# Optimization experiments

Hardware: AMD Instinct MI355X
Metric: run time of the kernel (lower is better)

Reference implementation:

```python
import jax, jax.numpy as jnp
import numpy as np


def setup_inputs() -> dict:
    key = jax.random.key(0)
    kK, kQ = jax.random.split(key)
    B, S, D = 8, 2048, 512
    K = jax.random.normal(kK, (B, S, D), dtype=jnp.float32)
    Q = jax.random.normal(kQ, (B, S, D), dtype=jnp.float32)
    return {"K": K, "Q": Q}


def reference(K, Q):
    # K: [B, S_k, D], Q: [B, S_q, D]
    S_q = Q.shape[1]
    S_k = K.shape[1]
    # Causal mask: -inf strictly above the diagonal (k=1), as in np.triu(..., k=1)
    mask = jnp.where(jnp.triu(jnp.ones((S_q, S_k), dtype=bool), k=1), -jnp.inf, 0.0).astype(jnp.float32)
    # NOTE: original scales by sqrt(window_size_keys) (seq len), and adds mask BEFORE scaling.
    logits = (jnp.einsum('bqd,bkd->bqk', Q, K) + mask) / jnp.sqrt(jnp.float32(S_k))
    return jax.nn.softmax(logits, axis=-1)
```

## Files before the change

kernel.cpp:

```cpp
#include <hip/hip_runtime.h>
#include <hip/hip_bf16.h>
#include <math.h>

#define B_SZ 8
#define SEQ 2048
#define DIM 512

typedef __attribute__((ext_vector_type(8))) short bf16x8;
typedef __attribute__((ext_vector_type(8))) unsigned short u16x8;
typedef __attribute__((ext_vector_type(4))) float f32x4;

#define GLOBAL_AS __attribute__((address_space(1)))
#define LDS_AS __attribute__((address_space(3)))

__device__ __forceinline__ unsigned short f2bf(float f) {
    unsigned int u = __builtin_bit_cast(unsigned int, f);
    u += 0x7fffu + ((u >> 16) & 1u);
    return (unsigned short)(u >> 16);
}

__device__ __forceinline__ void load_lds16(const void* g, void* l) {
    __builtin_amdgcn_global_load_lds((const GLOBAL_AS unsigned int*)g,
                                     (LDS_AS unsigned int*)l, 16, 0, 0);
}

__global__ __launch_bounds__(256)
void convert_kernel(const float* __restrict__ src, unsigned short* __restrict__ dst) {
    int i = blockIdx.x * 256 + threadIdx.x;
    const float4* s = (const float4*)src;
    float4 a = s[2 * i];
    float4 b = s[2 * i + 1];
    u16x8 o;
    o[0] = f2bf(a.x); o[1] = f2bf(a.y); o[2] = f2bf(a.z); o[3] = f2bf(a.w);
    o[4] = f2bf(b.x); o[5] = f2bf(b.y); o[6] = f2bf(b.z); o[7] = f2bf(b.w);
    ((u16x8*)dst)[i] = o;
}

#define BM 128
#define BK 32
__global__ __launch_bounds__(256)
void logits_mfma(const unsigned short* __restrict__ Qb, const unsigned short* __restrict__ Kb,
                 float* __restrict__ out) {
    const int tk = blockIdx.x, tq = blockIdx.y, b = blockIdx.z;
    if (tk > tq) return;

    __shared__ __align__(16) unsigned short a_lds[BM * BK];
    __shared__ __align__(16) unsigned short b_lds[BM * BK];

    const int t = threadIdx.x;
    const int wave = t >> 6;
    const int lane = t & 63;
    const int l16 = lane & 15;
    const int quad = lane >> 4;
    const int wm = wave >> 1;
    const int wn = wave & 1;

    const unsigned short* Qrow = Qb + ((size_t)b * SEQ + (size_t)tq * BM) * DIM;
    const unsigned short* Krow = Kb + ((size_t)b * SEQ + (size_t)tk * BM) * DIM;

    const int sr = lane >> 2;
    const int kg = lane & 3;

    f32x4 acc[4][4];
#pragma unroll
    for (int i = 0; i < 4; i++)
#pragma unroll
        for (int j = 0; j < 4; j++) acc[i][j] = (f32x4){0.f, 0.f, 0.f, 0.f};

    for (int k0 = 0; k0 < DIM; k0 += BK) {
#pragma unroll
        for (int j = wave; j < 8; j += 4) {
            int row = j * 16 + sr;
            load_lds16(Qrow + (size_t)row * DIM + k0 + kg * 8, &a_lds[(j * 16) * BK]);
            load_lds16(Krow + (size_t)row * DIM + k0 + kg * 8, &b_lds[(j * 16) * BK]);
        }
        __syncthreads();

        bf16x8 af[4], bf[4];
#pragma unroll
        for (int mi = 0; mi < 4; mi++)
            af[mi] = *(const bf16x8*)&a_lds[(wm * 64 + mi * 16 + l16) * BK + quad * 8];
#pragma unroll
        for (int ni = 0; ni < 4; ni++)
            bf[ni] = *(const bf16x8*)&b_lds[(wn * 64 + ni * 16 + l16) * BK + quad * 8];
#pragma unroll
        for (int mi = 0; mi < 4; mi++)
#pragma unroll
            for (int ni = 0; ni < 4; ni++)
                acc[mi][ni] = __builtin_amdgcn_mfma_f32_16x16x32_bf16(af[mi], bf[ni], acc[mi][ni], 0, 0, 0);
        __syncthreads();
    }

    const float scale = 0.02209708691207961f;
    float* outb = out + (size_t)b * SEQ * SEQ;
#pragma unroll
    for (int mi = 0; mi < 4; mi++) {
#pragma unroll
        for (int ni = 0; ni < 4; ni++) {
            int col = tk * BM + wn * 64 + ni * 16 + l16;
#pragma unroll
            for (int r = 0; r < 4; r++) {
                int row = tq * BM + wm * 64 + mi * 16 + quad * 4 + r;
                outb[(size_t)row * SEQ + col] = acc[mi][ni][r] * scale;
            }
        }
    }
}

__global__ __launch_bounds__(256)
void softmax_kernel(float* __restrict__ out) {
    const int q = blockIdx.x & (SEQ - 1);
    const int b = blockIdx.x >> 11;
    float* row = out + ((size_t)b * SEQ + q) * SEQ;
    const int t = threadIdx.x;
    const int lane = t & 63;
    const int wave = t >> 6;
    const int n = q + 1;

    __shared__ float red[8];

    float4 v[2];
    float m = -INFINITY;
#pragma unroll
    for (int j = 0; j < 2; j++) {
        int k0 = (t + j * 256) * 4;
        if (k0 < n) {
            float4 x = *(const float4*)(row + k0);
            x.y = (k0 + 1 < n) ? x.y : -INFINITY;
            x.z = (k0 + 2 < n) ? x.z : -INFINITY;
            x.w = (k0 + 3 < n) ? x.w : -INFINITY;
            v[j] = x;
            m = fmaxf(m, fmaxf(fmaxf(x.x, x.y), fmaxf(x.z, x.w)));
        } else {
            v[j] = (float4){-INFINITY, -INFINITY, -INFINITY, -INFINITY};
        }
    }
#pragma unroll
    for (int off = 1; off < 64; off <<= 1) m = fmaxf(m, __shfl_xor(m, off));
    if (lane == 0) red[wave] = m;
    __syncthreads();
    m = fmaxf(fmaxf(red[0], red[1]), fmaxf(red[2], red[3]));

    float s = 0.f;
#pragma unroll
    for (int j = 0; j < 2; j++) {
        float4 e;
        e.x = __expf(v[j].x - m);
        e.y = __expf(v[j].y - m);
        e.z = __expf(v[j].z - m);
        e.w = __expf(v[j].w - m);
        v[j] = e;
        s += e.x + e.y + e.z + e.w;
    }
#pragma unroll
    for (int off = 1; off < 64; off <<= 1) s += __shfl_xor(s, off);
    if (lane == 0) red[4 + wave] = s;
    __syncthreads();
    s = red[4] + red[5] + red[6] + red[7];
    const float inv = 1.0f / s;

#pragma unroll
    for (int j = 0; j < 2; j++) {
        int k0 = (t + j * 256) * 4;
        float4 e = v[j];
        e.x *= inv; e.y *= inv; e.z *= inv; e.w *= inv;
        *(float4*)(row + k0) = e;
    }
}

#define TS 64
#define DC 128
#define LSTRIDE (DC + 8)
__global__ __launch_bounds__(256)
void logits_fallback(const float* __restrict__ Q, const float* __restrict__ K,
                     float* __restrict__ out) {
    const int tk = blockIdx.x, tq = blockIdx.y, b = blockIdx.z;
    if (tk > tq) return;
    __shared__ __align__(16) unsigned short qs[TS * LSTRIDE];
    __shared__ __align__(16) unsigned short ks[TS * LSTRIDE];
    const int t = threadIdx.x;
    const int wave = t >> 6, lane = t & 63, l16 = lane & 15, quad = lane >> 4;
    const float* Qb = Q + ((size_t)b * SEQ + (size_t)tq * TS) * DIM;
    const float* Kb = K + ((size_t)b * SEQ + (size_t)tk * TS) * DIM;
    f32x4 acc[4];
#pragma unroll
    for (int i = 0; i < 4; i++) acc[i] = (f32x4){0.f, 0.f, 0.f, 0.f};
    for (int c = 0; c < DIM; c += DC) {
        __syncthreads();
#pragma unroll
        for (int i = 0; i < 8; i++) {
            int idx = t + i * 256;
            int row = idx >> 5, c4 = idx & 31;
            float4 qv = *(const float4*)(Qb + row * DIM + c + c4 * 4);
            float4 kv = *(const float4*)(Kb + row * DIM + c + c4 * 4);
            ushort4 qh = { f2bf(qv.x), f2bf(qv.y), f2bf(qv.z), f2bf(qv.w) };
            ushort4 kh = { f2bf(kv.x), f2bf(kv.y), f2bf(kv.z), f2bf(kv.w) };
            *(ushort4*)&qs[row * LSTRIDE + c4 * 4] = qh;
            *(ushort4*)&ks[row * LSTRIDE + c4 * 4] = kh;
        }
        __syncthreads();
#pragma unroll
        for (int d = 0; d < DC; d += 32) {
            bf16x8 afrag = *(const bf16x8*)&qs[(wave * 16 + l16) * LSTRIDE + d + quad * 8];
#pragma unroll
            for (int nt = 0; nt < 4; nt++) {
                bf16x8 bfrag = *(const bf16x8*)&ks[(nt * 16 + l16) * LSTRIDE + d + quad * 8];
                acc[nt] = __builtin_amdgcn_mfma_f32_16x16x32_bf16(afrag, bfrag, acc[nt], 0, 0, 0);
            }
        }
    }
    const float scale = 0.02209708691207961f;
    float* outb = out + (size_t)b * SEQ * SEQ;
#pragma unroll
    for (int nt = 0; nt < 4; nt++) {
        int col = tk * TS + nt * 16 + l16;
#pragma unroll
        for (int r = 0; r < 4; r++) {
            int row = tq * TS + wave * 16 + quad * 4 + r;
            outb[(size_t)row * SEQ + col] = acc[nt][r] * scale;
        }
    }
}

extern "C" void kernel_launch(void* const* d_in, const int* in_sizes, int n_in,
                              void* d_out, int out_size, void* d_ws, size_t ws_size,
                              hipStream_t stream) {
    const float* Kp = (const float*)d_in[0];
    const float* Qp = (const float*)d_in[1];
    float* out = (float*)d_out;

    const size_t nElem = (size_t)B_SZ * SEQ * DIM;
    if (ws_size >= 2 * nElem * sizeof(unsigned short)) {
        unsigned short* Qbf = (unsigned short*)d_ws;
        unsigned short* Kbf = Qbf + nElem;
        int cblocks = (int)(nElem / 8 / 256);
        convert_kernel<<<dim3(cblocks), dim3(256), 0, stream>>>(Qp, Qbf);
        convert_kernel<<<dim3(cblocks), dim3(256), 0, stream>>>(Kp, Kbf);
        logits_mfma<<<dim3(SEQ / BM, SEQ / BM, B_SZ), dim3(256), 0, stream>>>(Qbf, Kbf, out);
    } else {
        logits_fallback<<<dim3(SEQ / TS, SEQ / TS, B_SZ), dim3(256), 0, stream>>>(Qp, Kp, out);
    }
    softmax_kernel<<<dim3(B_SZ * SEQ), dim3(256), 0, stream>>>(out);
}
```

Baseline: 242.8 us.

## Fuse exp and row-sum into GEMM epilogue, replace softmax with scale pass

```diff
diff --git a/kernel.cpp b/kernel.cpp
--- a/kernel.cpp
+++ b/kernel.cpp
@@ -25,8 +25,20 @@
 }
 
 __global__ __launch_bounds__(256)
-void convert_kernel(const float* __restrict__ src, unsigned short* __restrict__ dst) {
-    int i = blockIdx.x * 256 + threadIdx.x;
+void convert_kernel(const float* __restrict__ Q, const float* __restrict__ K,
+                    unsigned short* __restrict__ Qb, unsigned short* __restrict__ Kb,
+                    float* __restrict__ sums) {
+    const int half = (int)(((size_t)B_SZ * SEQ * DIM) / 8 / 256);
+    const int bid = blockIdx.x;
+    const int gi = bid * 256 + threadIdx.x;
+    if (gi < B_SZ * SEQ) sums[gi] = 0.f;
+
+    const float* src;
+    unsigned short* dst;
+    int i;
+    if (bid < half) { src = Q; dst = Qb; i = gi; }
+    else            { src = K; dst = Kb; i = gi - half * 256; }
+
     const float4* s = (const float4*)src;
     float4 a = s[2 * i];
     float4 b = s[2 * i + 1];
@@ -39,15 +51,26 @@
 #define BM 128
 #define BK 32
 __global__ __launch_bounds__(256)
-void logits_mfma(const unsigned short* __restrict__ Qb, const unsigned short* __restrict__ Kb,
-                 float* __restrict__ out) {
+void logits_exp_mfma(const unsigned short* __restrict__ Qb, const unsigned short* __restrict__ Kb,
+                     float* __restrict__ out, float* __restrict__ sums) {
     const int tk = blockIdx.x, tq = blockIdx.y, b = blockIdx.z;
-    if (tk > tq) return;
+    float* outb = out + (size_t)b * SEQ * SEQ;
+    const int t = threadIdx.x;
+
+    if (tk > tq) {
+        const int r0 = t >> 5;
+        const int c4 = t & 31;
+        const float4 z = {0.f, 0.f, 0.f, 0.f};
+        float* base = outb + (size_t)(tq * BM) * SEQ + tk * BM;
+#pragma unroll
+        for (int it = 0; it < 16; ++it)
+            *(float4*)(base + (size_t)(it * 8 + r0) * SEQ + c4 * 4) = z;
+        return;
+    }
 
     __shared__ __align__(16) unsigned short a_lds[BM * BK];
     __shared__ __align__(16) unsigned short b_lds[BM * BK];
 
-    const int t = threadIdx.x;
     const int wave = t >> 6;
     const int lane = t & 63;
     const int l16 = lane & 15;
@@ -76,33 +99,119 @@
         }
         __syncthreads();
 
-        bf16x8 af[4], bf[4];
+        bf16x8 af[4], bfr[4];
 #pragma unroll
         for (int mi = 0; mi < 4; mi++)
             af[mi] = *(const bf16x8*)&a_lds[(wm * 64 + mi * 16 + l16) * BK + quad * 8];
 #pragma unroll
         for (int ni = 0; ni < 4; ni++)
-            bf[ni] = *(const bf16x8*)&b_lds[(wn * 64 + ni * 16 + l16) * BK + quad * 8];
+            bfr[ni] = *(const bf16x8*)&b_lds[(wn * 64 + ni * 16 + l16) * BK + quad * 8];
 #pragma unroll
         for (int mi = 0; mi < 4; mi++)
 #pragma unroll
             for (int ni = 0; ni < 4; ni++)
-                acc[mi][ni] = __builtin_amdgcn_mfma_f32_16x16x32_bf16(af[mi], bf[ni], acc[mi][ni], 0, 0, 0);
+                acc[mi][ni] = __builtin_amdgcn_mfma_f32_16x16x32_bf16(af[mi], bfr[ni], acc[mi][ni], 0, 0, 0);
         __syncthreads();
     }
 
+    const float scale = 0.02209708691207961f;
+    const bool diag = (tk == tq);
+    float* sums_b = sums + (size_t)b * SEQ;
+
+#pragma unroll
+    for (int mi = 0; mi < 4; mi++) {
+#pragma unroll
+        for (int r = 0; r < 4; r++) {
+            const int row_l = wm * 64 + mi * 16 + quad * 4 + r;
+            const int row = tq * BM + row_l;
+            float rsum = 0.f;
+#pragma unroll
+            for (int ni = 0; ni < 4; ni++) {
+                const int col = tk * BM + wn * 64 + ni * 16 + l16;
+                float e;
+                if (diag && col > row) e = 0.f;
+                else e = __expf(acc[mi][ni][r] * scale);
+                outb[(size_t)row * SEQ + col] = e;
+                rsum += e;
+            }
+            rsum += __shfl_xor(rsum, 1);
+            rsum += __shfl_xor(rsum, 2);
+            rsum += __shfl_xor(rsum, 4);
+            rsum += __shfl_xor(rsum, 8);
+            if (l16 == 0) atomicAdd(&sums_b[row], rsum);
+        }
+    }
+}
+
+__global__ __launch_bounds__(256)
+void scale_kernel(float* __restrict__ out, const float* __restrict__ sums) {
+    const int q = blockIdx.x & (SEQ - 1);
+    const int b = blockIdx.x >> 11;
+    float* row = out + ((size_t)b * SEQ + q) * SEQ;
+    const float inv = 1.0f / sums[blockIdx.x];
+    const int n = q + 1;
+    const int t = threadIdx.x;
+#pragma unroll
+    for (int j = 0; j < 2; ++j) {
+        int k0 = (t + j * 256) * 4;
+        if (k0 < n) {
+            float4 x = *(const float4*)(row + k0);
+            x.x *= inv; x.y *= inv; x.z *= inv; x.w *= inv;
+            *(float4*)(row + k0) = x;
+        }
+    }
+}
+
+#define TS 64
+#define DC 128
+#define LSTRIDE (DC + 8)
+__global__ __launch_bounds__(256)
+void logits_fallback(const float* __restrict__ Q, const float* __restrict__ K,
+                     float* __restrict__ out) {
+    const int tk = blockIdx.x, tq = blockIdx.y, b = blockIdx.z;
+    if (tk > tq) return;
+    __shared__ __align__(16) unsigned short qs[TS * LSTRIDE];
+    __shared__ __align__(16) unsigned short ks[TS * LSTRIDE];
+    const int t = threadIdx.x;
+    const int wave = t >> 6, lane = t & 63, l16 = lane & 15, quad = lane >> 4;
+    const float* Qb = Q + ((size_t)b * SEQ + (size_t)tq * TS) * DIM;
+    const float* Kb = K + ((size_t)b * SEQ + (size_t)tk * TS) * DIM;
+    f32x4 acc[4];
+#pragma unroll
+    for (int i = 0; i < 4; i++) acc[i] = (f32x4){0.f, 0.f, 0.f, 0.f};
+    for (int c = 0; c < DIM; c += DC) {
+        __syncthreads();
+#pragma unroll
+        for (int i = 0; i < 8; i++) {
+            int idx = t + i * 256;
+            int row = idx >> 5, c4 = idx & 31;
+            float4 qv = *(const float4*)(Qb + row * DIM + c + c4 * 4);
+            float4 kv = *(const float4*)(Kb + row * DIM + c + c4 * 4);
+            ushort4 qh = { f2bf(qv.x), f2bf(qv.y), f2bf(qv.z), f2bf(qv.w) };
+            ushort4 kh = { f2bf(kv.x), f2bf(kv.y), f2bf(kv.z), f2bf(kv.w) };
+            *(ushort4*)&qs[row * LSTRIDE + c4 * 4] = qh;
+            *(ushort4*)&ks[row * LSTRIDE + c4 * 4] = kh;
+        }
+        __syncthreads();
+#pragma unroll
+        for (int d = 0; d < DC; d += 32) {
+            bf16x8 afrag = *(const bf16x8*)&qs[(wave * 16 + l16) * LSTRIDE + d + quad * 8];
+#pragma unroll
+            for (int nt = 0; nt < 4; nt++) {
+                bf16x8 bfrag = *(const bf16x8*)&ks[(nt * 16 + l16) * LSTRIDE + d + quad * 8];
+                acc[nt] = __builtin_amdgcn_mfma_f32_16x16x32_bf16(afrag, bfrag, acc[nt], 0, 0, 0);
+            }
+        }
+    }
     const float scale = 0.02209708691207961f;
     float* outb = out + (size_t)b * SEQ * SEQ;
 #pragma unroll
-    for (int mi = 0; mi < 4; mi++) {
-#pragma unroll
-        for (int ni = 0; ni < 4; ni++) {
-            int col = tk * BM + wn * 64 + ni * 16 + l16;
-#pragma unroll
-            for (int r = 0; r < 4; r++) {
-                int row = tq * BM + wm * 64 + mi * 16 + quad * 4 + r;
-                outb[(size_t)row * SEQ + col] = acc[mi][ni][r] * scale;
-            }
+    for (int nt = 0; nt < 4; nt++) {
+        int col = tk * TS + nt * 16 + l16;
+#pragma unroll
+        for (int r = 0; r < 4; r++) {
+            int row = tq * TS + wave * 16 + quad * 4 + r;
+            outb[(size_t)row * SEQ + col] = acc[nt][r] * scale;
         }
     }
 }
@@ -168,60 +277,6 @@
     }
 }
 
-#define TS 64
-#define DC 128
-#define LSTRIDE (DC + 8)
-__global__ __launch_bounds__(256)
-void logits_fallback(const float* __restrict__ Q, const float* __restrict__ K,
-                     float* __restrict__ out) {
-    const int tk = blockIdx.x, tq = blockIdx.y, b = blockIdx.z;
-    if (tk > tq) return;
-    __shared__ __align__(16) unsigned short qs[TS * LSTRIDE];
-    __shared__ __align__(16) unsigned short ks[TS * LSTRIDE];
-    const int t = threadIdx.x;
-    const int wave = t >> 6, lane = t & 63, l16 = lane & 15, quad = lane >> 4;
-    const float* Qb = Q + ((size_t)b * SEQ + (size_t)tq * TS) * DIM;
-    const float* Kb = K + ((size_t)b * SEQ + (size_t)tk * TS) * DIM;
-    f32x4 acc[4];
-#pragma unroll
-    for (int i = 0; i < 4; i++) acc[i] = (f32x4){0.f, 0.f, 0.f, 0.f};
-    for (int c = 0; c < DIM; c += DC) {
-        __syncthreads();
-#pragma unroll
-        for (int i = 0; i < 8; i++) {
-            int idx = t + i * 256;
-            int row = idx >> 5, c4 = idx & 31;
-            float4 qv = *(const float4*)(Qb + row * DIM + c + c4 * 4);
-            float4 kv = *(const float4*)(Kb + row * DIM + c + c4 * 4);
-            ushort4 qh = { f2bf(qv.x), f2bf(qv.y), f2bf(qv.z), f2bf(qv.w) };
-            ushort4 kh = { f2bf(kv.x), f2bf(kv.y), f2bf(kv.z), f2bf(kv.w) };
-            *(ushort4*)&qs[row * LSTRIDE + c4 * 4] = qh;
-            *(ushort4*)&ks[row * LSTRIDE + c4 * 4] = kh;
-        }
-        __syncthreads();
-#pragma unroll
-        for (int d = 0; d < DC; d += 32) {
-            bf16x8 afrag = *(const bf16x8*)&qs[(wave * 16 + l16) * LSTRIDE + d + quad * 8];
-#pragma unroll
-            for (int nt = 0; nt < 4; nt++) {
-                bf16x8 bfrag = *(const bf16x8*)&ks[(nt * 16 + l16) * LSTRIDE + d + quad * 8];
-                acc[nt] = __builtin_amdgcn_mfma_f32_16x16x32_bf16(afrag, bfrag, acc[nt], 0, 0, 0);
-            }
-        }
-    }
-    const float scale = 0.02209708691207961f;
-    float* outb = out + (size_t)b * SEQ * SEQ;
-#pragma unroll
-    for (int nt = 0; nt < 4; nt++) {
-        int col = tk * TS + nt * 16 + l16;
-#pragma unroll
-        for (int r = 0; r < 4; r++) {
-            int row = tq * TS + wave * 16 + quad * 4 + r;
-            outb[(size_t)row * SEQ + col] = acc[nt][r] * scale;
-        }
-    }
-}
-
 extern "C" void kernel_launch(void* const* d_in, const int* in_sizes, int n_in,
                               void* d_out, int out_size, void* d_ws, size_t ws_size,
                               hipStream_t stream) {
@@ -230,15 +285,19 @@
     float* out = (float*)d_out;
 
     const size_t nElem = (size_t)B_SZ * SEQ * DIM;
-    if (ws_size >= 2 * nElem * sizeof(unsigned short)) {
+    const size_t bfBytes = nElem * sizeof(unsigned short);
+    const size_t sumsBytes = (size_t)B_SZ * SEQ * sizeof(float);
+
+    if (ws_size >= 2 * bfBytes + sumsBytes) {
         unsigned short* Qbf = (unsigned short*)d_ws;
         unsigned short* Kbf = Qbf + nElem;
-        int cblocks = (int)(nElem / 8 / 256);
-        convert_kernel<<<dim3(cblocks), dim3(256), 0, stream>>>(Qp, Qbf);
-        convert_kernel<<<dim3(cblocks), dim3(256), 0, stream>>>(Kp, Kbf);
-        logits_mfma<<<dim3(SEQ / BM, SEQ / BM, B_SZ), dim3(256), 0, stream>>>(Qbf, Kbf, out);
+        float* sums = (float*)((char*)d_ws + 2 * bfBytes);
+        const int half = (int)(nElem / 8 / 256);
+        convert_kernel<<<dim3(2 * half), dim3(256), 0, stream>>>(Qp, Kp, Qbf, Kbf, sums);
+        logits_exp_mfma<<<dim3(SEQ / BM, SEQ / BM, B_SZ), dim3(256), 0, stream>>>(Qbf, Kbf, out, sums);
+        scale_kernel<<<dim3(B_SZ * SEQ), dim3(256), 0, stream>>>(out, sums);
     } else {
         logits_fallback<<<dim3(SEQ / TS, SEQ / TS, B_SZ), dim3(256), 0, stream>>>(Qp, Kp, out);
-    }
-    softmax_kernel<<<dim3(B_SZ * SEQ), dim3(256), 0, stream>>>(out);
-}
+        softmax_kernel<<<dim3(B_SZ * SEQ), dim3(256), 0, stream>>>(out);
+    }
+}
```

Result: slower. 247.9 us (+2.1%).
